# Kernel optimization log

Hardware: AMD Instinct MI355X
Metric: run time of the kernel (lower is better)

Reference implementation:

```python
import jax, jax.numpy as jnp
import numpy as np

B, S, NX, H = 8, 1024, 1024, 16
HD = NX // H  # head dim = 64
MASKED_BIAS = -10000.0


def setup_inputs() -> dict:
    key = jax.random.key(0)
    ks = jax.random.split(key, 6)
    return {
        "x": jax.random.normal(ks[0], (B, S, NX), dtype=jnp.float32),
        "query": jax.random.normal(ks[1], (B, S, NX), dtype=jnp.float32),
        "c_attn_w": jax.random.normal(ks[2], (NX, 3 * NX), dtype=jnp.float32) * 0.02,
        "c_attn_b": jnp.zeros((3 * NX,), dtype=jnp.float32),
        "c_proj_w": jax.random.normal(ks[3], (NX, NX), dtype=jnp.float32) * 0.02,
        "c_proj_b": jnp.zeros((NX,), dtype=jnp.float32),
    }


def _split_heads(t):
    # [B, S, NX] -> [B, H, S, HD]
    b, s, _ = t.shape
    return t.reshape(b, s, H, HD).transpose(0, 2, 1, 3)


def reference(x, query, c_attn_w, c_attn_b, c_proj_w, c_proj_b):
    # Conv1D: y = x @ W + b
    kv = x @ c_attn_w + c_attn_b          # [B,S,3NX]; use key/value slices
    qy = query @ c_attn_w + c_attn_b      # [B,S,3NX]; use query slice
    q = _split_heads(qy[..., :NX])                     # [B,H,S,HD]
    k = _split_heads(kv[..., NX:2 * NX])               # [B,H,S,HD]
    v = _split_heads(kv[..., 2 * NX:])                 # [B,H,S,HD]

    w = jnp.einsum("bhqd,bhkd->bhqk", q, k) / jnp.sqrt(jnp.float32(HD))
    causal = jnp.tril(jnp.ones((S, S), dtype=bool))[None, None]
    w = jnp.where(causal, w, jnp.float32(MASKED_BIAS))
    w = jax.nn.softmax(w, axis=-1)
    a = jnp.einsum("bhqk,bhkd->bhqd", w, v)            # [B,H,S,HD]
    a = a.transpose(0, 2, 1, 3).reshape(B, S, NX)      # merge heads
    return a @ c_proj_w + c_proj_b
```

## Files before the change

### kernel.cpp

```cpp
#include <hip/hip_runtime.h>
#include <cstdint>
#include <cstddef>

#define Bb   8
#define Ss   1024
#define NXx  1024
#define Hh   16
#define HDd  64
#define Mm   (Bb*Ss)

typedef __bf16 bf16x8 __attribute__((ext_vector_type(8)));
typedef float  f32x4  __attribute__((ext_vector_type(4)));

__device__ __forceinline__ unsigned short f2bf(float f) {
    union { float f; unsigned int u; } v; v.f = f;
    return (unsigned short)((v.u + 0x8000u) >> 16);
}

__device__ __forceinline__ unsigned cvt_pk_bf16(float lo, float hi) {
    unsigned r;
    asm("v_cvt_pk_bf16_f32 %0, %1, %2" : "=v"(r) : "v"(lo), "v"(hi));
    return r;
}

__device__ __forceinline__ void load_lds16(const unsigned short* g, unsigned short* lds_base) {
    __builtin_amdgcn_global_load_lds(
        (const __attribute__((address_space(1))) void*)g,
        (__attribute__((address_space(3))) void*)lds_base, 16, 0, 0);
}

__global__ __launch_bounds__(256) void prep(
    const float* __restrict__ x, const float* __restrict__ query,
    const float* __restrict__ caw, const float* __restrict__ cpw,
    unsigned short* __restrict__ xb, unsigned short* __restrict__ qb,
    unsigned short* __restrict__ Wt, unsigned short* __restrict__ Pt)
{
    __shared__ float tile[32][33];
    const int bid = blockIdx.x;
    const int tid = threadIdx.x;

    if (bid < 16384) {
        const float* in = (bid < 8192) ? x : query;
        unsigned short* out = (bid < 8192) ? xb : qb;
        const int i = ((bid & 8191) * 256 + tid) * 4;
        const float4 v = *(const float4*)(in + i);
        unsigned long long p = (unsigned long long)f2bf(v.x)
            | ((unsigned long long)f2bf(v.y) << 16)
            | ((unsigned long long)f2bf(v.z) << 32)
            | ((unsigned long long)f2bf(v.w) << 48);
        *(unsigned long long*)(out + i) = p;
        return;
    }

    const float* in;
    unsigned short* out;
    int C, t;
    if (bid < 16384 + 3072) { in = caw; out = Wt; C = 3072; t = bid - 16384; }
    else                    { in = cpw; out = Pt; C = 1024; t = bid - 19456; }
    const int ntx = C >> 5;
    const int c0 = (t % ntx) * 32, r0 = (t / ntx) * 32;
    const int tx = tid & 31, ty = tid >> 5;
    for (int i = ty; i < 32; i += 8)
        tile[i][tx] = in[(size_t)(r0 + i) * C + c0 + tx];
    __syncthreads();
    for (int i = ty; i < 32; i += 8)
        out[(size_t)(c0 + i) * 1024 + r0 + tx] = f2bf(tile[tx][i]);
}

__global__ __launch_bounds__(256) void gemm128(
    const unsigned short* __restrict__ Ax,
    const unsigned short* __restrict__ Aq,
    const unsigned short* __restrict__ Bt,
    const float* __restrict__ bias,
    int K, int mode,
    unsigned short* __restrict__ out_q,
    unsigned short* __restrict__ out_k,
    unsigned short* __restrict__ out_v,
    float* __restrict__ out_f)
{
    __shared__ unsigned short smem[16384];
    unsigned short (*As)[64] = (unsigned short (*)[64])(smem);
    unsigned short (*Bs)[64] = (unsigned short (*)[64])(smem + 8192);

    const int tid  = threadIdx.x;
    const int w    = tid >> 6;
    const int lane = tid & 63;

    const int nx   = (mode == 0) ? 24 : 8;
    const int nxh  = nx >> 1;
    const int n    = blockIdx.x;
    const int xcd  = n & 7;
    const int sgrp = n >> 3;
    const int m0   = ((xcd >> 1) * 16 + sgrp / nxh) * 128;
    const int n0   = ((xcd & 1) * nxh + sgrp % nxh) * 128;
    const int region = n0 >> 10;
    const unsigned short* A = (mode == 0 && region == 0) ? Aq : Ax;

    const int wm   = (w >> 1) * 64;
    const int wn   = (w & 1) * 64;
    const int lrow = lane & 15;
    const int quad = lane >> 4;

    f32x4 acc[4][4] = {};

    const int rr   = lane >> 3;
    const int scol = (((lane & 7) ^ (lane >> 3)) << 3);
    const unsigned short* Ag = A  + (size_t)(m0 + w * 32 + rr) * K + scol;
    const unsigned short* Bg = Bt + (size_t)(n0 + w * 32 + rr) * K + scol;
    unsigned short* ldsA = smem + (w * 32) * 64;
    unsigned short* ldsB = smem + 8192 + (w * 32) * 64;

    const int swz = lrow & 7;

    for (int k0 = 0; k0 < K; k0 += 64) {
        __syncthreads();
#pragma unroll
        for (int c = 0; c < 4; ++c) {
            load_lds16(Ag + (size_t)(c * 8) * K + k0, ldsA + c * 512);
            load_lds16(Bg + (size_t)(c * 8) * K + k0, ldsB + c * 512);
        }
        __syncthreads();
#pragma unroll
        for (int kk = 0; kk < 2; ++kk) {
            bf16x8 af[4], bfr[4];
            const int pc = (((kk * 4 + quad) ^ swz) << 3);
#pragma unroll
            for (int i = 0; i < 4; ++i) {
                af[i]  = *(const bf16x8*)&As[wm + i * 16 + lrow][pc];
                bfr[i] = *(const bf16x8*)&Bs[wn + i * 16 + lrow][pc];
            }
#pragma unroll
            for (int i = 0; i < 4; ++i)
#pragma unroll
                for (int j = 0; j < 4; ++j)
                    acc[i][j] = __builtin_amdgcn_mfma_f32_16x16x32_bf16(af[i], bfr[j], acc[i][j], 0, 0, 0);
        }
    }

    __syncthreads();

    if (mode == 1) {
#pragma unroll
        for (int i = 0; i < 4; ++i)
#pragma unroll
            for (int j = 0; j < 4; ++j) {
                const int ncol = n0 + wn + j * 16 + lrow;
                const float bv = bias[ncol];
#pragma unroll
                for (int r = 0; r < 4; ++r) {
                    const int mrow = m0 + wm + i * 16 + quad * 4 + r;
                    out_f[(size_t)mrow * NXx + ncol] = acc[i][j][r] + bv;
                }
            }
        return;
    }

    unsigned short* ep = smem + w * 2048;

    if (region != 2) {
        unsigned short* outp = (region == 0) ? out_q : out_k;
#pragma unroll
        for (int j = 0; j < 4; ++j) {
            const float bv = bias[n0 + wn + j * 16 + lrow];
#pragma unroll
            for (int i = 0; i < 4; ++i)
#pragma unroll
                for (int r = 0; r < 4; ++r)
                    ep[(i * 16 + quad * 4 + r) * 24 + lrow] = f2bf(acc[i][j][r] + bv);
#pragma unroll
            for (int t = 0; t < 2; ++t) {
                const int c    = t * 64 + lane;
                const int row  = c >> 1, ch = (c & 1) * 8;
                const int mrow = m0 + wm + row;
                const int cc   = (n0 + wn + j * 16 + ch) & (NXx - 1);
                const int hh   = cc >> 6, dd = cc & 63;
                const int bh   = (mrow >> 10) * Hh + hh;
                const int ss   = mrow & (Ss - 1);
                *(uint4*)&outp[((size_t)bh * Ss + ss) * HDd + dd] =
                    *(const uint4*)&ep[row * 24 + ch];
            }
        }
    } else {
#pragma unroll
        for (int j = 0; j < 4; ++j) {
            const float bv = bias[n0 + wn + j * 16 + lrow];
#pragma unroll
            for (int i = 0; i < 4; ++i)
#pragma unroll
                for (int r = 0; r < 4; ++r)
                    ep[lrow * 72 + i * 16 + quad * 4 + r] = f2bf(acc[i][j][r] + bv);
#pragma unroll
            for (int t = 0; t < 2; ++t) {
                const int c    = t * 64 + lane;
                const int col  = c >> 3, rc = (c & 7) * 8;
                const int cc   = (n0 + wn + j * 16 + col) & (NXx - 1);
                const int hh   = cc >> 6, dd = cc & 63;
                const int mrow = m0 + wm + rc;
                const int bh   = (mrow >> 10) * Hh + hh;
                const int ss   = mrow & (Ss - 1);
                *(uint4*)&out_v[((size_t)bh * HDd + dd) * Ss + ss] =
                    *(const uint4*)&ep[col * 72 + rc];
            }
        }
    }
}

__global__ __launch_bounds__(512, 4) void gemm256(
    const unsigned short* __restrict__ Ax,
    const unsigned short* __restrict__ Aq,
    const unsigned short* __restrict__ Bt,
    const float* __restrict__ bias,
    unsigned short* __restrict__ out_q,
    unsigned short* __restrict__ out_k,
    unsigned short* __restrict__ out_v)
{
    __shared__ unsigned short lds[36864];

    const int tid  = threadIdx.x;
    const int w    = tid >> 6;
    const int lane = tid & 63;
    const int wm   = (w >> 1) * 64;
    const int wn   = (w & 1) * 64;
    const int lrow = lane & 15;
    const int quad = lane >> 4;
    const int ph   = (quad ^ (lrow & 3) ^ (lrow >> 2)) & 3;

    const int n    = blockIdx.x;
    const int xcd  = n & 7;
    const int sg   = n >> 3;
    const int mi   = (xcd >> 1) * 8 + sg / 12;
    const int ni   = (xcd & 1) * 12 + sg % 12;
    const int m0   = mi << 8;
    const int n0   = ni << 7;
    const int region = n0 >> 10;
    const unsigned short* A = (region == 0) ? Aq : Ax;

    const int srow = lane >> 2;
    const int scol = (((lane & 3) ^ (srow & 3) ^ ((srow >> 2) & 3)) << 3);
    const unsigned short* pA0 = A  + (size_t)(m0 + w * 32 + srow) * 1024 + scol;
    const unsigned short* pA1 = A  + (size_t)(m0 + w * 32 + 16 + srow) * 1024 + scol;
    const unsigned short* pB0 = Bt + (size_t)(n0 + w * 16 + srow) * 1024 + scol;

    f32x4 acc[4][4] = {};

#pragma unroll
    for (int p = 0; p < 2; ++p) {
        const int bb = p * 12288;
        load_lds16(pA0, lds + bb + w * 1024);
        load_lds16(pA1, lds + bb + w * 1024 + 512);
        load_lds16(pB0, lds + bb + 8192 + w * 512);
        pA0 += 32; pA1 += 32; pB0 += 32;
    }

    int cbuf = 0;
    int sbuf = 2;
#pragma unroll 1
    for (int t = 0; t < 32; ++t) {
        __builtin_amdgcn_s_barrier();
        asm volatile("" ::: "memory");
        if (t <= 29) {
            const int bb = sbuf * 12288;
            load_lds16(pA0, lds + bb + w * 1024);
            load_lds16(pA1, lds + bb + w * 1024 + 512);
            load_lds16(pB0, lds + bb + 8192 + w * 512);
            pA0 += 32; pA1 += 32; pB0 += 32;
            asm volatile("s_waitcnt vmcnt(6)" ::: "memory");
        } else if (t == 30) {
            asm volatile("s_waitcnt vmcnt(3)" ::: "memory");
        } else {
            asm volatile("s_waitcnt vmcnt(0)" ::: "memory");
        }
        __builtin_amdgcn_s_barrier();
        asm volatile("" ::: "memory");

        const int rA = cbuf * 12288 + (wm + lrow) * 32 + ph * 8;
        const int rB = cbuf * 12288 + 8192 + (wn + lrow) * 32 + ph * 8;
        bf16x8 af[4], bq[4];
#pragma unroll
        for (int i = 0; i < 4; ++i) af[i] = *(const bf16x8*)&lds[rA + i * 512];
#pragma unroll
        for (int j = 0; j < 4; ++j) bq[j] = *(const bf16x8*)&lds[rB + j * 512];
        __builtin_amdgcn_s_setprio(1);
#pragma unroll
        for (int i = 0; i < 4; ++i)
#pragma unroll
            for (int j = 0; j < 4; ++j)
                acc[i][j] = __builtin_amdgcn_mfma_f32_16x16x32_bf16(af[i], bq[j], acc[i][j], 0, 0, 0);
        __builtin_amdgcn_s_setprio(0);

        cbuf = (cbuf == 2) ? 0 : cbuf + 1;
        sbuf = (sbuf == 2) ? 0 : sbuf + 1;
    }

    __syncthreads();

    unsigned short* ep = lds + w * 2048;

    if (region != 2) {
        unsigned short* outp = (region == 0) ? out_q : out_k;
        const float sc = (region == 0) ? 0.125f : 1.0f;
#pragma unroll
        for (int j = 0; j < 4; ++j) {
            const float bv = bias[n0 + wn + j * 16 + lrow];
#pragma unroll
            for (int i = 0; i < 4; ++i)
#pragma unroll
                for (int r = 0; r < 4; ++r)
                    ep[(i * 16 + quad * 4 + r) * 24 + lrow] = f2bf((acc[i][j][r] + bv) * sc);
#pragma unroll
            for (int tt = 0; tt < 2; ++tt) {
                const int c    = tt * 64 + lane;
                const int row  = c >> 1, ch = (c & 1) * 8;
                const int mrow = m0 + wm + row;
                const int cc   = (n0 + wn + j * 16 + ch) & (NXx - 1);
                const int hh   = cc >> 6, dd = cc & 63;
                const int bh   = (mrow >> 10) * Hh + hh;
                const int ss   = mrow & (Ss - 1);
                *(uint4*)&outp[((size_t)bh * Ss + ss) * HDd + dd] =
                    *(const uint4*)&ep[row * 24 + ch];
            }
        }
    } else {
#pragma unroll
        for (int j = 0; j < 4; ++j) {
            const float bv = bias[n0 + wn + j * 16 + lrow];
#pragma unroll
            for (int i = 0; i < 4; ++i)
#pragma unroll
                for (int r = 0; r < 4; ++r)
                    ep[lrow * 72 + i * 16 + quad * 4 + r] = f2bf(acc[i][j][r] + bv);
#pragma unroll
            for (int tt = 0; tt < 2; ++tt) {
                const int c    = tt * 64 + lane;
                const int col  = c >> 3, rc = (c & 7) * 8;
                const int cc   = (n0 + wn + j * 16 + col) & (NXx - 1);
                const int hh   = cc >> 6, dd = cc & 63;
                const int mrow = m0 + wm + rc;
                const int bh   = (mrow >> 10) * Hh + hh;
                const int ss   = mrow & (Ss - 1);
                *(uint4*)&out_v[((size_t)bh * HDd + dd) * Ss + ss] =
                    *(const uint4*)&ep[col * 72 + rc];
            }
        }
    }
}

__global__ __launch_bounds__(512) void flash_attn(
    const unsigned short* __restrict__ Qh,
    const unsigned short* __restrict__ Kh,
    const unsigned short* __restrict__ Vt,
    unsigned short* __restrict__ about)
{
    __shared__ unsigned short Ks[3][64][64];
    __shared__ unsigned short Vs[3][64][64];
    __shared__ unsigned short Pl[8][32][72];

    const int tid  = threadIdx.x;
    const int w    = tid >> 6;
    const int lane = tid & 63;
    const int bh   = blockIdx.x & 127;
    const int prg  = blockIdx.x >> 7;
    const int b    = bh >> 4, h = bh & 15;
    const int lrow = lane & 15;
    const int quad = lane >> 4;

    const unsigned short* Qb = Qh + (size_t)bh * Ss * HDd;
    const unsigned short* Kb = Kh + (size_t)bh * Ss * HDd;
    const unsigned short* Vb = Vt + (size_t)bh * HDd * Ss;

    const int sr = lane >> 3;
    const int lc = (((lane & 7) ^ sr) << 3);

    const int swz = lrow & 7;
    const int ca = ((quad ^ swz) << 3);
    const int cb = (((4 + quad) ^ swz) << 3);

    const int nkt0 = 4 * prg + 4;
    int qw = prg * 256 + w * 32;

    bf16x8 aq[2][2];
#pragma unroll
    for (int g = 0; g < 2; ++g)
#pragma unroll
        for (int c = 0; c < 2; ++c)
            aq[g][c] = *(const bf16x8*)(Qb + (size_t)(qw + g * 16 + lrow) * HDd + c * 32 + quad * 8);

    f32x4 O[2][4] = {};
    float lsum[2] = { 0.f, 0.f };

#pragma unroll
    for (int p = 0; p < 2; ++p) {
        load_lds16(Kb + (size_t)(p * 64 + w * 8 + sr) * HDd + lc, &Ks[p][w * 8][0]);
        load_lds16(Vb + (size_t)(w * 8 + sr) * Ss + p * 64 + lc,  &Vs[p][w * 8][0]);
    }

    int cbuf = 0;
    int sbuf = 2;
#pragma unroll 1
    for (int it = 0; it < 20; ++it) {
        __builtin_amdgcn_s_barrier();
        asm volatile("" ::: "memory");
        if (it <= 17) {
            const int itn = it + 2;
            const int k0n = (itn >= nkt0 ? itn - nkt0 : itn) * 64;
            load_lds16(Kb + (size_t)(k0n + w * 8 + sr) * HDd + lc, &Ks[sbuf][w * 8][0]);
            load_lds16(Vb + (size_t)(w * 8 + sr) * Ss + k0n + lc,  &Vs[sbuf][w * 8][0]);
            asm volatile("s_waitcnt vmcnt(4)" ::: "memory");
        } else if (it == 18) {
            asm volatile("s_waitcnt vmcnt(2)" ::: "memory");
        } else {
            asm volatile("s_waitcnt vmcnt(0)" ::: "memory");
        }
        __builtin_amdgcn_s_barrier();
        asm volatile("" ::: "memory");

        if (it == nkt0) {
#pragma unroll
            for (int g = 0; g < 2; ++g) {
                float l = lsum[g];
                l += __shfl_xor(l, 16);
                l += __shfl_xor(l, 32);
                const float inv = 1.0f / l;
#pragma unroll
                for (int r = 0; r < 4; ++r) {
                    const float invr = __shfl(inv, quad * 4 + r);
                    const int q = qw + g * 16 + quad * 4 + r;
                    const size_t base = ((size_t)b * Ss + q) * NXx + h * HDd;
#pragma unroll
                    for (int f = 0; f < 4; ++f)
                        about[base + f * 16 + lrow] = f2bf(O[g][f][r] * invr);
                }
            }
            qw = (3 - prg) * 256 + w * 32;
#pragma unroll
            for (int g = 0; g < 2; ++g)
#pragma unroll
                for (int c = 0; c < 2; ++c)
                    aq[g][c] = *(const bf16x8*)(Qb + (size_t)(qw + g * 16 + lrow) * HDd + c * 32 + quad * 8);
#pragma unroll
            for (int g = 0; g < 2; ++g) {
                lsum[g] = 0.f;
#pragma unroll
                for (int f = 0; f < 4; ++f) O[g][f] = (f32x4){0.f, 0.f, 0.f, 0.f};
            }
        }

        const int k0 = (it >= nkt0 ? it - nkt0 : it) * 64;
        if (k0 <= qw + 31) {
            f32x4 st[2][4] = {};
#pragma unroll
            for (int j = 0; j < 4; ++j) {
                const bf16x8 kf0 = *(const bf16x8*)&Ks[cbuf][j * 16 + lrow][ca];
                const bf16x8 kf1 = *(const bf16x8*)&Ks[cbuf][j * 16 + lrow][cb];
                st[0][j] = __builtin_amdgcn_mfma_f32_16x16x32_bf16(kf0, aq[0][0], st[0][j], 0, 0, 0);
                st[0][j] = __builtin_amdgcn_mfma_f32_16x16x32_bf16(kf1, aq[0][1], st[0][j], 0, 0, 0);
                st[1][j] = __builtin_amdgcn_mfma_f32_16x16x32_bf16(kf0, aq[1][0], st[1][j], 0, 0, 0);
                st[1][j] = __builtin_amdgcn_mfma_f32_16x16x32_bf16(kf1, aq[1][1], st[1][j], 0, 0, 0);
            }

            const bool needMask = (k0 + 63 > qw);
#pragma unroll
            for (int g = 0; g < 2; ++g) {
                const int qg = qw + g * 16 + lrow;
#pragma unroll
                for (int j = 0; j < 4; ++j) {
                    const int kbase = k0 + j * 16 + quad * 4;
                    float e0 = __expf(st[g][j][0]);
                    float e1 = __expf(st[g][j][1]);
                    float e2 = __expf(st[g][j][2]);
                    float e3 = __expf(st[g][j][3]);
                    if (needMask) {
                        if (kbase     > qg) e0 = 0.f;
                        if (kbase + 1 > qg) e1 = 0.f;
                        if (kbase + 2 > qg) e2 = 0.f;
                        if (kbase + 3 > qg) e3 = 0.f;
                    }
                    lsum[g] += (e0 + e1) + (e2 + e3);
                    uint2 pk;
                    pk.x = cvt_pk_bf16(e0, e1);
                    pk.y = cvt_pk_bf16(e2, e3);
                    *(uint2*)&Pl[w][g * 16 + lrow][j * 16 + quad * 4] = pk;
                }
            }

            bf16x8 ap[2][2];
#pragma unroll
            for (int g = 0; g < 2; ++g)
#pragma unroll
                for (int c = 0; c < 2; ++c)
                    ap[g][c] = *(const bf16x8*)&Pl[w][g * 16 + lrow][c * 32 + quad * 8];
#pragma unroll
            for (int f = 0; f < 4; ++f) {
                const bf16x8 vf0 = *(const bf16x8*)&Vs[cbuf][f * 16 + lrow][ca];
                const bf16x8 vf1 = *(const bf16x8*)&Vs[cbuf][f * 16 + lrow][cb];
                O[0][f] = __builtin_amdgcn_mfma_f32_16x16x32_bf16(ap[0][0], vf0, O[0][f], 0, 0, 0);
                O[0][f] = __builtin_amdgcn_mfma_f32_16x16x32_bf16(ap[0][1], vf1, O[0][f], 0, 0, 0);
                O[1][f] = __builtin_amdgcn_mfma_f32_16x16x32_bf16(ap[1][0], vf0, O[1][f], 0, 0, 0);
                O[1][f] = __builtin_amdgcn_mfma_f32_16x16x32_bf16(ap[1][1], vf1, O[1][f], 0, 0, 0);
            }
        }

        cbuf = (cbuf == 2) ? 0 : cbuf + 1;
        sbuf = (sbuf == 2) ? 0 : sbuf + 1;
    }

#pragma unroll
    for (int g = 0; g < 2; ++g) {
        float l = lsum[g];
        l += __shfl_xor(l, 16);
        l += __shfl_xor(l, 32);
        const float inv = 1.0f / l;
#pragma unroll
        for (int r = 0; r < 4; ++r) {
            const float invr = __shfl(inv, quad * 4 + r);
            const int q = qw + g * 16 + quad * 4 + r;
            const size_t base = ((size_t)b * Ss + q) * NXx + h * HDd;
#pragma unroll
            for (int f = 0; f < 4; ++f)
                about[base + f * 16 + lrow] = f2bf(O[g][f][r] * invr);
        }
    }
}

extern "C" void kernel_launch(void* const* d_in, const int* in_sizes, int n_in,
                              void* d_out, int out_size, void* d_ws, size_t ws_size,
                              hipStream_t stream) {
    const float* x        = (const float*)d_in[0];
    const float* query    = (const float*)d_in[1];
    const float* c_attn_w = (const float*)d_in[2];
    const float* c_attn_b = (const float*)d_in[3];
    const float* c_proj_w = (const float*)d_in[4];
    const float* c_proj_b = (const float*)d_in[5];
    float* out = (float*)d_out;

    const size_t nTok = (size_t)Mm * NXx;
    char* ws = (char*)d_ws;
    unsigned short* xb    = (unsigned short*)ws;                 ws += nTok * 2;
    unsigned short* qb    = (unsigned short*)ws;                 ws += nTok * 2;
    unsigned short* Wt    = (unsigned short*)ws;                 ws += (size_t)3 * NXx * NXx * 2;
    unsigned short* Pt    = (unsigned short*)ws;                 ws += (size_t)NXx * NXx * 2;
    unsigned short* Qh    = (unsigned short*)ws;                 ws += nTok * 2;
    unsigned short* Kh    = (unsigned short*)ws;                 ws += nTok * 2;
    unsigned short* Vt    = (unsigned short*)ws;                 ws += nTok * 2;
    unsigned short* about = (unsigned short*)ws;                 ws += nTok * 2;
    if ((size_t)(ws - (char*)d_ws) > ws_size) return;

    prep<<<20480, 256, 0, stream>>>(x, query, c_attn_w, c_proj_w, xb, qb, Wt, Pt);

    gemm256<<<768, 512, 0, stream>>>(xb, qb, Wt, c_attn_b, Qh, Kh, Vt);

    flash_attn<<<256, 512, 0, stream>>>(Qh, Kh, Vt, about);

    gemm128<<<dim3(8 * 64), 256, 0, stream>>>(about, nullptr, Pt, c_proj_b, NXx, 1,
                                              nullptr, nullptr, nullptr, out);
}
```

Measured before the change: 254.2 us.

## Use single-barrier triple-buffered pipelines and replace output projection GEMM kernel

In the QKV GEMM and flash attention loops, the second barrier per iteration is removed. The vmcnt wait moves to the end of each iteration, after the compute, so the next tile's loads can overlap with MFMA work under a single barrier. The old 128x128 output projection GEMM is replaced by a new 512-thread triple-buffered kernel using the same swizzled direct-to-LDS loading scheme. This cuts synchronisation overhead, but correctness now depends on the ordering of the three-buffer ring together with one barrier per step.

```diff
diff --git a/kernel.cpp b/kernel.cpp
--- a/kernel.cpp
+++ b/kernel.cpp
@@ -67,144 +67,6 @@
         out[(size_t)(c0 + i) * 1024 + r0 + tx] = f2bf(tile[tx][i]);
 }
 
-__global__ __launch_bounds__(256) void gemm128(
-    const unsigned short* __restrict__ Ax,
-    const unsigned short* __restrict__ Aq,
-    const unsigned short* __restrict__ Bt,
-    const float* __restrict__ bias,
-    int K, int mode,
-    unsigned short* __restrict__ out_q,
-    unsigned short* __restrict__ out_k,
-    unsigned short* __restrict__ out_v,
-    float* __restrict__ out_f)
-{
-    __shared__ unsigned short smem[16384];
-    unsigned short (*As)[64] = (unsigned short (*)[64])(smem);
-    unsigned short (*Bs)[64] = (unsigned short (*)[64])(smem + 8192);
-
-    const int tid  = threadIdx.x;
-    const int w    = tid >> 6;
-    const int lane = tid & 63;
-
-    const int nx   = (mode == 0) ? 24 : 8;
-    const int nxh  = nx >> 1;
-    const int n    = blockIdx.x;
-    const int xcd  = n & 7;
-    const int sgrp = n >> 3;
-    const int m0   = ((xcd >> 1) * 16 + sgrp / nxh) * 128;
-    const int n0   = ((xcd & 1) * nxh + sgrp % nxh) * 128;
-    const int region = n0 >> 10;
-    const unsigned short* A = (mode == 0 && region == 0) ? Aq : Ax;
-
-    const int wm   = (w >> 1) * 64;
-    const int wn   = (w & 1) * 64;
-    const int lrow = lane & 15;
-    const int quad = lane >> 4;
-
-    f32x4 acc[4][4] = {};
-
-    const int rr   = lane >> 3;
-    const int scol = (((lane & 7) ^ (lane >> 3)) << 3);
-    const unsigned short* Ag = A  + (size_t)(m0 + w * 32 + rr) * K + scol;
-    const unsigned short* Bg = Bt + (size_t)(n0 + w * 32 + rr) * K + scol;
-    unsigned short* ldsA = smem + (w * 32) * 64;
-    unsigned short* ldsB = smem + 8192 + (w * 32) * 64;
-
-    const int swz = lrow & 7;
-
-    for (int k0 = 0; k0 < K; k0 += 64) {
-        __syncthreads();
-#pragma unroll
-        for (int c = 0; c < 4; ++c) {
-            load_lds16(Ag + (size_t)(c * 8) * K + k0, ldsA + c * 512);
-            load_lds16(Bg + (size_t)(c * 8) * K + k0, ldsB + c * 512);
-        }
-        __syncthreads();
-#pragma unroll
-        for (int kk = 0; kk < 2; ++kk) {
-            bf16x8 af[4], bfr[4];
-            const int pc = (((kk * 4 + quad) ^ swz) << 3);
-#pragma unroll
-            for (int i = 0; i < 4; ++i) {
-                af[i]  = *(const bf16x8*)&As[wm + i * 16 + lrow][pc];
-                bfr[i] = *(const bf16x8*)&Bs[wn + i * 16 + lrow][pc];
-            }
-#pragma unroll
-            for (int i = 0; i < 4; ++i)
-#pragma unroll
-                for (int j = 0; j < 4; ++j)
-                    acc[i][j] = __builtin_amdgcn_mfma_f32_16x16x32_bf16(af[i], bfr[j], acc[i][j], 0, 0, 0);
-        }
-    }
-
-    __syncthreads();
-
-    if (mode == 1) {
-#pragma unroll
-        for (int i = 0; i < 4; ++i)
-#pragma unroll
-            for (int j = 0; j < 4; ++j) {
-                const int ncol = n0 + wn + j * 16 + lrow;
-                const float bv = bias[ncol];
-#pragma unroll
-                for (int r = 0; r < 4; ++r) {
-                    const int mrow = m0 + wm + i * 16 + quad * 4 + r;
-                    out_f[(size_t)mrow * NXx + ncol] = acc[i][j][r] + bv;
-                }
-            }
-        return;
-    }
-
-    unsigned short* ep = smem + w * 2048;
-
-    if (region != 2) {
-        unsigned short* outp = (region == 0) ? out_q : out_k;
-#pragma unroll
-        for (int j = 0; j < 4; ++j) {
-            const float bv = bias[n0 + wn + j * 16 + lrow];
-#pragma unroll
-            for (int i = 0; i < 4; ++i)
-#pragma unroll
-                for (int r = 0; r < 4; ++r)
-                    ep[(i * 16 + quad * 4 + r) * 24 + lrow] = f2bf(acc[i][j][r] + bv);
-#pragma unroll
-            for (int t = 0; t < 2; ++t) {
-                const int c    = t * 64 + lane;
-                const int row  = c >> 1, ch = (c & 1) * 8;
-                const int mrow = m0 + wm + row;
-                const int cc   = (n0 + wn + j * 16 + ch) & (NXx - 1);
-                const int hh   = cc >> 6, dd = cc & 63;
-                const int bh   = (mrow >> 10) * Hh + hh;
-                const int ss   = mrow & (Ss - 1);
-                *(uint4*)&outp[((size_t)bh * Ss + ss) * HDd + dd] =
-                    *(const uint4*)&ep[row * 24 + ch];
-            }
-        }
-    } else {
-#pragma unroll
-        for (int j = 0; j < 4; ++j) {
-            const float bv = bias[n0 + wn + j * 16 + lrow];
-#pragma unroll
-            for (int i = 0; i < 4; ++i)
-#pragma unroll
-                for (int r = 0; r < 4; ++r)
-                    ep[lrow * 72 + i * 16 + quad * 4 + r] = f2bf(acc[i][j][r] + bv);
-#pragma unroll
-            for (int t = 0; t < 2; ++t) {
-                const int c    = t * 64 + lane;
-                const int col  = c >> 3, rc = (c & 7) * 8;
-                const int cc   = (n0 + wn + j * 16 + col) & (NXx - 1);
-                const int hh   = cc >> 6, dd = cc & 63;
-                const int mrow = m0 + wm + rc;
-                const int bh   = (mrow >> 10) * Hh + hh;
-                const int ss   = mrow & (Ss - 1);
-                *(uint4*)&out_v[((size_t)bh * HDd + dd) * Ss + ss] =
-                    *(const uint4*)&ep[col * 72 + rc];
-            }
-        }
-    }
-}
-
 __global__ __launch_bounds__(512, 4) void gemm256(
     const unsigned short* __restrict__ Ax,
     const unsigned short* __restrict__ Aq,
@@ -251,6 +113,7 @@
         load_lds16(pB0, lds + bb + 8192 + w * 512);
         pA0 += 32; pA1 += 32; pB0 += 32;
     }
+    asm volatile("s_waitcnt vmcnt(3)" ::: "memory");
 
     int cbuf = 0;
     int sbuf = 2;
@@ -264,14 +127,7 @@
             load_lds16(pA1, lds + bb + w * 1024 + 512);
             load_lds16(pB0, lds + bb + 8192 + w * 512);
             pA0 += 32; pA1 += 32; pB0 += 32;
-            asm volatile("s_waitcnt vmcnt(6)" ::: "memory");
-        } else if (t == 30) {
-            asm volatile("s_waitcnt vmcnt(3)" ::: "memory");
-        } else {
-            asm volatile("s_waitcnt vmcnt(0)" ::: "memory");
-        }
-        __builtin_amdgcn_s_barrier();
-        asm volatile("" ::: "memory");
+        }
 
         const int rA = cbuf * 12288 + (wm + lrow) * 32 + ph * 8;
         const int rB = cbuf * 12288 + 8192 + (wn + lrow) * 32 + ph * 8;
@@ -287,6 +143,9 @@
             for (int j = 0; j < 4; ++j)
                 acc[i][j] = __builtin_amdgcn_mfma_f32_16x16x32_bf16(af[i], bq[j], acc[i][j], 0, 0, 0);
         __builtin_amdgcn_s_setprio(0);
+
+        if (t <= 29)      asm volatile("s_waitcnt vmcnt(3)" ::: "memory");
+        else if (t == 30) asm volatile("s_waitcnt vmcnt(0)" ::: "memory");
 
         cbuf = (cbuf == 2) ? 0 : cbuf + 1;
         sbuf = (sbuf == 2) ? 0 : sbuf + 1;
@@ -345,6 +204,95 @@
     }
 }
 
+__global__ __launch_bounds__(512, 4) void gemmp(
+    const unsigned short* __restrict__ A,
+    const unsigned short* __restrict__ Bt,
+    const float* __restrict__ bias,
+    float* __restrict__ out_f)
+{
+    __shared__ unsigned short lds[24576];
+
+    const int tid  = threadIdx.x;
+    const int w    = tid >> 6;
+    const int lane = tid & 63;
+    const int wm   = (w >> 1) * 32;
+    const int wn   = (w & 1) * 64;
+    const int lrow = lane & 15;
+    const int quad = lane >> 4;
+    const int ph   = (quad ^ (lrow & 3) ^ (lrow >> 2)) & 3;
+
+    const int n    = blockIdx.x;
+    const int xcd  = n & 7;
+    const int sg   = n >> 3;
+    const int mi   = (xcd >> 1) * 16 + sg / 4;
+    const int ni   = (xcd & 1) * 4 + (sg & 3);
+    const int m0   = mi << 7;
+    const int n0   = ni << 7;
+
+    const int srow = lane >> 2;
+    const int scol = (((lane & 3) ^ (srow & 3) ^ ((srow >> 2) & 3)) << 3);
+    const unsigned short* pA0 = A  + (size_t)(m0 + w * 16 + srow) * 1024 + scol;
+    const unsigned short* pB0 = Bt + (size_t)(n0 + w * 16 + srow) * 1024 + scol;
+
+    f32x4 acc[2][4] = {};
+
+#pragma unroll
+    for (int p = 0; p < 2; ++p) {
+        const int bb = p * 8192;
+        load_lds16(pA0, lds + bb + w * 512);
+        load_lds16(pB0, lds + bb + 4096 + w * 512);
+        pA0 += 32; pB0 += 32;
+    }
+    asm volatile("s_waitcnt vmcnt(2)" ::: "memory");
+
+    int cbuf = 0, sbuf = 2;
+#pragma unroll 1
+    for (int t = 0; t < 32; ++t) {
+        __builtin_amdgcn_s_barrier();
+        asm volatile("" ::: "memory");
+        if (t <= 29) {
+            const int bb = sbuf * 8192;
+            load_lds16(pA0, lds + bb + w * 512);
+            load_lds16(pB0, lds + bb + 4096 + w * 512);
+            pA0 += 32; pB0 += 32;
+        }
+
+        const int rA = cbuf * 8192 + (wm + lrow) * 32 + ph * 8;
+        const int rB = cbuf * 8192 + 4096 + (wn + lrow) * 32 + ph * 8;
+        bf16x8 af[2], bq[4];
+#pragma unroll
+        for (int i = 0; i < 2; ++i) af[i] = *(const bf16x8*)&lds[rA + i * 512];
+#pragma unroll
+        for (int j = 0; j < 4; ++j) bq[j] = *(const bf16x8*)&lds[rB + j * 512];
+        __builtin_amdgcn_s_setprio(1);
+#pragma unroll
+        for (int i = 0; i < 2; ++i)
+#pragma unroll
+            for (int j = 0; j < 4; ++j)
+                acc[i][j] = __builtin_amdgcn_mfma_f32_16x16x32_bf16(af[i], bq[j], acc[i][j], 0, 0, 0);
+        __builtin_amdgcn_s_setprio(0);
+
+        if (t <= 29)      asm volatile("s_waitcnt vmcnt(2)" ::: "memory");
+        else if (t == 30) asm volatile("s_waitcnt vmcnt(0)" ::: "memory");
+
+        cbuf = (cbuf == 2) ? 0 : cbuf + 1;
+        sbuf = (sbuf == 2) ? 0 : sbuf + 1;
+    }
+
+#pragma unroll
+    for (int i = 0; i < 2; ++i)
+#pragma unroll
+        for (int j = 0; j < 4; ++j) {
+            const int ncol = n0 + wn + j * 16 + lrow;
+            const float bv = bias[ncol];
+#pragma unroll
+            for (int r = 0; r < 4; ++r) {
+                const int mrow = m0 + wm + i * 16 + quad * 4 + r;
+                out_f[(size_t)mrow * NXx + ncol] = acc[i][j][r] + bv;
+            }
+        }
+}
+
 __global__ __launch_bounds__(512) void flash_attn(
     const unsigned short* __restrict__ Qh,
     const unsigned short* __restrict__ Kh,
@@ -393,9 +341,9 @@
         load_lds16(Kb + (size_t)(p * 64 + w * 8 + sr) * HDd + lc, &Ks[p][w * 8][0]);
         load_lds16(Vb + (size_t)(w * 8 + sr) * Ss + p * 64 + lc,  &Vs[p][w * 8][0]);
     }
-
-    int cbuf = 0;
-    int sbuf = 2;
+    asm volatile("s_waitcnt vmcnt(2)" ::: "memory");
+
+    int cbuf = 0, sbuf = 2;
 #pragma unroll 1
     for (int it = 0; it < 20; ++it) {
         __builtin_amdgcn_s_barrier();
@@ -405,14 +353,7 @@
             const int k0n = (itn >= nkt0 ? itn - nkt0 : itn) * 64;
             load_lds16(Kb + (size_t)(k0n + w * 8 + sr) * HDd + lc, &Ks[sbuf][w * 8][0]);
             load_lds16(Vb + (size_t)(w * 8 + sr) * Ss + k0n + lc,  &Vs[sbuf][w * 8][0]);
-            asm volatile("s_waitcnt vmcnt(4)" ::: "memory");
-        } else if (it == 18) {
-            asm volatile("s_waitcnt vmcnt(2)" ::: "memory");
-        } else {
-            asm volatile("s_waitcnt vmcnt(0)" ::: "memory");
-        }
-        __builtin_amdgcn_s_barrier();
-        asm volatile("" ::: "memory");
+        }
 
         if (it == nkt0) {
 #pragma unroll
@@ -500,6 +441,9 @@
             }
         }
 
+        if (it <= 17)      asm volatile("s_waitcnt vmcnt(2)" ::: "memory");
+        else if (it == 18) asm volatile("s_waitcnt vmcnt(0)" ::: "memory");
+
         cbuf = (cbuf == 2) ? 0 : cbuf + 1;
         sbuf = (sbuf == 2) ? 0 : sbuf + 1;
     }
@@ -551,6 +495,5 @@
 
     flash_attn<<<256, 512, 0, stream>>>(Qh, Kh, Vt, about);
 
-    gemm128<<<dim3(8 * 64), 256, 0, stream>>>(about, nullptr, Pt, c_proj_b, NXx, 1,
-                                              nullptr, nullptr, nullptr, out);
-}
+    gemmp<<<512, 512, 0, stream>>>(about, Pt, c_proj_b, out);
+}
```

Result: slower. 262.2 us (+3.1%).
